# Kernel optimization log

Hardware: AMD Instinct MI355X
Metric: run time of the kernel (lower is better)

The kernel has to match this reference:

```python
import jax, jax.numpy as jnp
import numpy as np

DT = 0.01
NT = 2000
B = 16384


def setup_inputs() -> dict:
    key = jax.random.key(0)
    k1, k2 = jax.random.split(key)
    x0 = jax.random.normal(k1, (B, 3), dtype=jnp.float32)
    p = jax.random.uniform(k2, (3,), dtype=jnp.float32) * 10.0  # matches torch.rand(3)*10
    return {"x0": x0, "p": p}


def _yp(X, p):
    # Lorenz RHS, X: [B, 3]
    x, y, z = X[:, 0], X[:, 1], X[:, 2]
    return jnp.stack([p[0] * (y - x), x * (p[1] - z) - y, x * y - p[2] * z], axis=1)


def reference(x0, p):
    dt = jnp.float32(DT)

    def step(Xi, _):
        k1 = _yp(Xi, p)
        k2 = _yp(Xi + dt / 2 * k1, p)
        k3 = _yp(Xi + dt / 2 * k2, p)
        k4 = _yp(Xi + dt * k3, p)
        Xn = Xi + dt / 6 * (k1 + 2 * k2 + 2 * k3 + k4)
        return Xn, Xn

    _, traj = jax.lax.scan(step, x0, None, length=NT)  # [NT, B, 3]
    X = jnp.concatenate([x0[None], traj], axis=0)      # [NT+1, B, 3]
    return jnp.transpose(X, (1, 2, 0))                  # [B, 3, NT+1]
```

## Files before the change

kernel.cpp:

```cpp
#include <hip/hip_runtime.h>


#define TROWS  2001
#define ROWS   64
#define LROWS  65
#define TT     64

#define FMA(a,b,c) __builtin_fmaf((a),(b),(c))

__global__ __launch_bounds__(192) void lorenz_rk4(
    const float* __restrict__ x0,
    const float* __restrict__ p,
    float* __restrict__ out)
{
#pragma clang fp contract(off)
    __shared__ float buf[2][3][TT][LROWS];

    const int tid  = threadIdx.x;
    const int lane = tid & 63;
    const int b0   = blockIdx.x * ROWS;

    if (tid < 64) {
        const float p0  = p[0], p1 = p[1], p2n = -p[2];
        const float h1 = 0.01f;
        const float h2 = 0.01f / 2.0f;
        const float h6 = 0.01f / 6.0f;
        const int b = b0 + lane;
        float x = x0[3*b + 0], y = x0[3*b + 1], z = x0[3*b + 2];

        {
            size_t g = (size_t)b * (3 * TROWS);
            out[g] = x; out[g + TROWS] = y; out[g + 2*TROWS] = z;
        }

#define STEP() do {                                                          \
        float k1x = p0 * (y - x);                                            \
        float k1y = FMA(x, p1 - z, -y);                                      \
        float k1z = FMA(p2n, z, x * y);                                      \
        float ax = FMA(h2,k1x,x), ay = FMA(h2,k1y,y), az = FMA(h2,k1z,z);    \
        float k2x = p0 * (ay - ax);                                          \
        float k2y = FMA(ax, p1 - az, -ay);                                   \
        float k2z = FMA(p2n, az, ax * ay);                                   \
        float bx = FMA(h2,k2x,x), by = FMA(h2,k2y,y), bz = FMA(h2,k2z,z);    \
        float k3x = p0 * (by - bx);                                          \
        float k3y = FMA(bx, p1 - bz, -by);                                   \
        float k3z = FMA(p2n, bz, bx * by);                                   \
        float cx = FMA(h1,k3x,x), cy = FMA(h1,k3y,y), cz = FMA(h1,k3z,z);    \
        float k4x = p0 * (cy - cx);                                          \
        float k4y = FMA(cx, p1 - cz, -cy);                                   \
        float k4z = FMA(p2n, cz, cx * cy);                                   \
        float sx = FMA(2.0f,k2x,k1x); sx = FMA(2.0f,k3x,sx); sx += k4x;      \
        float sy = FMA(2.0f,k2y,k1y); sy = FMA(2.0f,k3y,sy); sy += k4y;      \
        float sz = FMA(2.0f,k2z,k1z); sz = FMA(2.0f,k3z,sz); sz += k4z;      \
        x = FMA(h6,sx,x); y = FMA(h6,sy,y); z = FMA(h6,sz,z);                \
    } while (0)

#pragma unroll 7
        for (int tl = 0; tl < 63; ++tl) {
            STEP();
            buf[0][0][tl][lane] = x;
            buf[0][1][tl][lane] = y;
            buf[0][2][tl][lane] = z;
        }
        __syncthreads();

        for (int k = 1; k <= 30; ++k) {
            float* bb = &buf[k & 1][0][0][0];
#pragma unroll 8
            for (int tl = 0; tl < TT; ++tl) {
                STEP();
                bb[              tl*LROWS + lane] = x;
                bb[  TT*LROWS  + tl*LROWS + lane] = y;
                bb[2*TT*LROWS  + tl*LROWS + lane] = z;
            }
            __syncthreads();
        }

#pragma unroll
        for (int tl = 0; tl < 17; ++tl) {
            STEP();
            buf[1][0][tl][lane] = x;
            buf[1][1][tl][lane] = y;
            buf[1][2][tl][lane] = z;
        }
        __syncthreads();
#undef STEP
    } else {
        const int w     = (tid >> 6) - 1;
        const int rbase = w * 32;
        const int t     = lane;

        __syncthreads();
        {
            const float* bb = &buf[0][0][0][0];
            if (t < 63) {
                size_t g = (size_t)(b0 + rbase) * (3 * TROWS) + 1 + t;
#pragma unroll 4
                for (int r = rbase; r < rbase + 32; ++r) {
                    out[g]             = bb[              t*LROWS + r];
                    out[g +     TROWS] = bb[  TT*LROWS  + t*LROWS + r];
                    out[g + 2 * TROWS] = bb[2*TT*LROWS  + t*LROWS + r];
                    g += (size_t)(3 * TROWS);
                }
            }
        }

        for (int k = 1; k <= 30; ++k) {
            __syncthreads();
            const float* bb = &buf[k & 1][0][0][0];
            size_t g = (size_t)(b0 + rbase) * (3 * TROWS) + (size_t)TT * k + t;
#pragma unroll 4
            for (int r = rbase; r < rbase + 32; ++r) {
                out[g]             = bb[              t*LROWS + r];
                out[g +     TROWS] = bb[  TT*LROWS  + t*LROWS + r];
                out[g + 2 * TROWS] = bb[2*TT*LROWS  + t*LROWS + r];
                g += (size_t)(3 * TROWS);
            }
        }

        __syncthreads();
        {
            const float* bb = &buf[1][0][0][0];
            if (t < 17) {
                size_t g = (size_t)(b0 + rbase) * (3 * TROWS) + 1984 + t;
#pragma unroll 4
                for (int r = rbase; r < rbase + 32; ++r) {
                    out[g]             = bb[              t*LROWS + r];
                    out[g +     TROWS] = bb[  TT*LROWS  + t*LROWS + r];
                    out[g + 2 * TROWS] = bb[2*TT*LROWS  + t*LROWS + r];
                    g += (size_t)(3 * TROWS);
                }
            }
        }
    }
}

extern "C" void kernel_launch(void* const* d_in, const int* in_sizes, int n_in,
                              void* d_out, int out_size, void* d_ws, size_t ws_size,
                              hipStream_t stream)
{
    const float* x0  = (const float*)d_in[0];
    const float* p   = (const float*)d_in[1];
    float*       out = (float*)d_out;

    const int B = in_sizes[0] / 3;
    const int nblocks = B / ROWS;

    lorenz_rk4<<<nblocks, 192, 0, stream>>>(x0, p, out);
}
```

Measured before the change: 175.1 us.

## Transpose LDS tile layout, enlarge time tiles, and write output with vectorized nontemporal stores

The shared staging buffer becomes row-major per batch element with 96 time steps per tile instead of 64, so the compute wave writes each element's trajectory contiguously. The writer waves then read four consecutive time steps from LDS and emit 4-wide nontemporal global stores. The aim is fewer, wider store instructions and less cache pollution on the large output write. The compute wave's LDS writes now land at a stride of 97 floats between lanes, which may cost more bank conflicts, and the f4 stores are only 4-byte aligned because of the odd row length of 2001.

```diff
diff --git a/kernel.cpp b/kernel.cpp
--- a/kernel.cpp
+++ b/kernel.cpp
@@ -3,35 +3,15 @@
 
 #define TROWS  2001
 #define ROWS   64
-#define LROWS  65
-#define TT     64
+#define T0TILE 63
+#define TTILE  96
+#define NTILE  20
+#define TAILN  17
+#define LSTR   97
+
+typedef float f4 __attribute__((ext_vector_type(4), aligned(4)));
 
 #define FMA(a,b,c) __builtin_fmaf((a),(b),(c))
-
-__global__ __launch_bounds__(192) void lorenz_rk4(
-    const float* __restrict__ x0,
-    const float* __restrict__ p,
-    float* __restrict__ out)
-{
-#pragma clang fp contract(off)
-    __shared__ float buf[2][3][TT][LROWS];
-
-    const int tid  = threadIdx.x;
-    const int lane = tid & 63;
-    const int b0   = blockIdx.x * ROWS;
-
-    if (tid < 64) {
-        const float p0  = p[0], p1 = p[1], p2n = -p[2];
-        const float h1 = 0.01f;
-        const float h2 = 0.01f / 2.0f;
-        const float h6 = 0.01f / 6.0f;
-        const int b = b0 + lane;
-        float x = x0[3*b + 0], y = x0[3*b + 1], z = x0[3*b + 2];
-
-        {
-            size_t g = (size_t)b * (3 * TROWS);
-            out[g] = x; out[g + TROWS] = y; out[g + 2*TROWS] = z;
-        }
 
 #define STEP() do {                                                          \
         float k1x = p0 * (y - x);                                            \
@@ -55,80 +35,111 @@
         x = FMA(h6,sx,x); y = FMA(h6,sy,y); z = FMA(h6,sz,z);                \
     } while (0)
 
+__global__ __launch_bounds__(192) void lorenz_rk4(
+    const float* __restrict__ x0,
+    const float* __restrict__ p,
+    float* __restrict__ out)
+{
+#pragma clang fp contract(off)
+    __shared__ float buf[2][3][ROWS][LSTR];
+
+    const int tid  = threadIdx.x;
+    const int lane = tid & 63;
+    const int b0   = blockIdx.x * ROWS;
+
+    if (tid < 64) {
+        const float p0 = p[0], p1 = p[1], p2n = -p[2];
+        const float h1 = 0.01f, h2 = 0.01f / 2.0f, h6 = 0.01f / 6.0f;
+        const int b = b0 + lane;
+        float x = x0[3*b + 0], y = x0[3*b + 1], z = x0[3*b + 2];
+
+        {
+            size_t g = (size_t)b * (3 * TROWS);
+            out[g] = x; out[g + TROWS] = y; out[g + 2*TROWS] = z;
+        }
+
+        float* r0 = &buf[0][0][lane][0];
 #pragma unroll 7
-        for (int tl = 0; tl < 63; ++tl) {
+        for (int tl = 0; tl < T0TILE; ++tl) {
             STEP();
-            buf[0][0][tl][lane] = x;
-            buf[0][1][tl][lane] = y;
-            buf[0][2][tl][lane] = z;
+            r0[tl]                 = x;
+            r0[tl +   ROWS*LSTR]   = y;
+            r0[tl + 2*ROWS*LSTR]   = z;
         }
         __syncthreads();
 
-        for (int k = 1; k <= 30; ++k) {
-            float* bb = &buf[k & 1][0][0][0];
+        for (int k = 1; k <= NTILE; ++k) {
+            float* rr = &buf[k & 1][0][lane][0];
 #pragma unroll 8
-            for (int tl = 0; tl < TT; ++tl) {
+            for (int tl = 0; tl < TTILE; ++tl) {
                 STEP();
-                bb[              tl*LROWS + lane] = x;
-                bb[  TT*LROWS  + tl*LROWS + lane] = y;
-                bb[2*TT*LROWS  + tl*LROWS + lane] = z;
+                rr[tl]                 = x;
+                rr[tl +   ROWS*LSTR]   = y;
+                rr[tl + 2*ROWS*LSTR]   = z;
             }
             __syncthreads();
         }
 
+        float* rt = &buf[1][0][lane][0];
 #pragma unroll
-        for (int tl = 0; tl < 17; ++tl) {
+        for (int tl = 0; tl < TAILN; ++tl) {
             STEP();
-            buf[1][0][tl][lane] = x;
-            buf[1][1][tl][lane] = y;
-            buf[1][2][tl][lane] = z;
+            rt[tl]                 = x;
+            rt[tl +   ROWS*LSTR]   = y;
+            rt[tl + 2*ROWS*LSTR]   = z;
         }
         __syncthreads();
-#undef STEP
     } else {
         const int w     = (tid >> 6) - 1;
         const int rbase = w * 32;
-        const int t     = lane;
 
         __syncthreads();
         {
-            const float* bb = &buf[0][0][0][0];
-            if (t < 63) {
-                size_t g = (size_t)(b0 + rbase) * (3 * TROWS) + 1 + t;
+            const int t = lane;
+            if (t < T0TILE) {
 #pragma unroll 4
                 for (int r = rbase; r < rbase + 32; ++r) {
-                    out[g]             = bb[              t*LROWS + r];
-                    out[g +     TROWS] = bb[  TT*LROWS  + t*LROWS + r];
-                    out[g + 2 * TROWS] = bb[2*TT*LROWS  + t*LROWS + r];
-                    g += (size_t)(3 * TROWS);
+                    size_t g = (size_t)(b0 + r) * (3 * TROWS) + 1 + t;
+                    __builtin_nontemporal_store(buf[0][0][r][t], &out[g]);
+                    __builtin_nontemporal_store(buf[0][1][r][t], &out[g + TROWS]);
+                    __builtin_nontemporal_store(buf[0][2][r][t], &out[g + 2*TROWS]);
                 }
             }
         }
 
-        for (int k = 1; k <= 30; ++k) {
+        for (int k = 1; k <= NTILE; ++k) {
             __syncthreads();
-            const float* bb = &buf[k & 1][0][0][0];
-            size_t g = (size_t)(b0 + rbase) * (3 * TROWS) + (size_t)TT * k + t;
+            const int cl  = lane & 31;
+            const int rof = lane >> 5;
+            if (cl < 24) {
+                const int tl0 = 4 * cl;
+                const size_t obase = (size_t)TTILE * k - 32 + tl0;
 #pragma unroll 4
-            for (int r = rbase; r < rbase + 32; ++r) {
-                out[g]             = bb[              t*LROWS + r];
-                out[g +     TROWS] = bb[  TT*LROWS  + t*LROWS + r];
-                out[g + 2 * TROWS] = bb[2*TT*LROWS  + t*LROWS + r];
-                g += (size_t)(3 * TROWS);
+                for (int rp = 0; rp < 16; ++rp) {
+                    const int r = rbase + 2*rp + rof;
+                    const float* q = &buf[k & 1][0][r][tl0];
+                    size_t g = (size_t)(b0 + r) * (3 * TROWS) + obase;
+#pragma unroll
+                    for (int pl = 0; pl < 3; ++pl) {
+                        f4 v = { q[0], q[1], q[2], q[3] };
+                        __builtin_nontemporal_store(v, (f4*)(out + g));
+                        q += ROWS * LSTR;
+                        g += TROWS;
+                    }
+                }
             }
         }
 
         __syncthreads();
         {
-            const float* bb = &buf[1][0][0][0];
-            if (t < 17) {
-                size_t g = (size_t)(b0 + rbase) * (3 * TROWS) + 1984 + t;
+            const int t = lane;
+            if (t < TAILN) {
 #pragma unroll 4
                 for (int r = rbase; r < rbase + 32; ++r) {
-                    out[g]             = bb[              t*LROWS + r];
-                    out[g +     TROWS] = bb[  TT*LROWS  + t*LROWS + r];
-                    out[g + 2 * TROWS] = bb[2*TT*LROWS  + t*LROWS + r];
-                    g += (size_t)(3 * TROWS);
+                    size_t g = (size_t)(b0 + r) * (3 * TROWS) + 1984 + t;
+                    __builtin_nontemporal_store(buf[1][0][r][t], &out[g]);
+                    __builtin_nontemporal_store(buf[1][1][r][t], &out[g + TROWS]);
+                    __builtin_nontemporal_store(buf[1][2][r][t], &out[g + 2*TROWS]);
                 }
             }
         }
```

Measured after the change: 185.1 us. 1.06x slower.
